# Optimization experiments

Hardware: AMD Instinct MI355X
Metric: run time of the kernel (lower is better)

The kernel has to match this reference:

```python
import jax, jax.numpy as jnp
import numpy as np

B, IN, H = 8192, 2048, 2048

def setup_inputs() -> dict:
    key = jax.random.key(0)
    k1, k2, k3, k4 = jax.random.split(key, 4)
    gate_bound = 1.0 / (IN + H)
    input_bound = 1.0 / IN
    return {
        "input": jax.random.normal(k1, (B, IN), dtype=jnp.float32),
        "state": jax.random.normal(k2, (B, H), dtype=jnp.float32),
        "gate_weights": jax.random.uniform(k3, (H, H + IN), dtype=jnp.float32, minval=-gate_bound, maxval=gate_bound),
        "gate_bias": jnp.full((H,), 0.5, dtype=jnp.float32),
        "weights_i": jax.random.uniform(k4, (H, IN), dtype=jnp.float32, minval=-input_bound, maxval=input_bound),
    }

def reference(input, state, gate_weights, gate_bias, weights_i):
    # concat_input: [B, IN+H]
    concat_input = jnp.concatenate([input, state], axis=1)
    # pre_gate_i = concat_input @ gate_weights.T + gate_bias : [B, H]
    pre_gate_i = jnp.einsum('bc,hc->bh', concat_input, gate_weights) + gate_bias
    # eval-mode noisy_hard_sigmoid == Hardtanh(0,1)
    gate_i = jnp.clip(pre_gate_i, 0.0, 1.0)
    # values_i = tanh(input @ weights_i.T) : [B, H]
    values_i = jnp.tanh(jnp.einsum('bi,hi->bh', input, weights_i))
    pre_h = state * (1.0 - gate_i) + values_i * gate_i
    # eval-mode noisy_relu == relu
    new_h = jax.nn.relu(pre_h)
    return (new_h, concat_input, pre_gate_i, gate_i, values_i, pre_h)
```

## Files before the change

### kernel.cpp

```cpp
#include <hip/hip_runtime.h>
#include <cstdint>
#include <cstddef>

#define B_SZ  8192
#define IN_SZ 2048
#define H_SZ  2048
#define KC_SZ 4096

typedef unsigned short ushort_t;
typedef __attribute__((ext_vector_type(8))) short bf16x8;
typedef __attribute__((ext_vector_type(4))) float floatx4;

__device__ __forceinline__ ushort_t f2bf(float f) {
  union { float f; unsigned u; } v; v.f = f;
  unsigned u = v.u;
  return (ushort_t)((u + 0x7FFFu + ((u >> 16) & 1u)) >> 16);
}

__device__ __forceinline__ void g2lds16(const void* g, void* l) {
  __builtin_amdgcn_global_load_lds(
      (const __attribute__((address_space(1))) unsigned int*)g,
      (__attribute__((address_space(3))) unsigned int*)l, 16, 0, 0);
}

__global__ void prep_concat(const float* __restrict__ in, const float* __restrict__ st,
                            float* __restrict__ cat, ushort_t* __restrict__ Abf) {
  size_t i4 = (size_t)blockIdx.x * blockDim.x + threadIdx.x;
  size_t row  = i4 >> 10;
  size_t col4 = i4 & 1023;
  float4 v;
  if (col4 < (IN_SZ / 4))
    v = ((const float4*)in)[row * (IN_SZ / 4) + col4];
  else
    v = ((const float4*)st)[row * (H_SZ / 4) + (col4 - IN_SZ / 4)];
  ((float4*)cat)[i4] = v;
  union { ushort_t u[4]; uint2 p; } pk;
  pk.u[0] = f2bf(v.x); pk.u[1] = f2bf(v.y); pk.u[2] = f2bf(v.z); pk.u[3] = f2bf(v.w);
  ((uint2*)Abf)[i4] = pk.p;
}

__global__ void prep_weights(const float* __restrict__ gw, const float* __restrict__ wi,
                             ushort_t* __restrict__ Wg, ushort_t* __restrict__ Wi) {
  size_t i4 = (size_t)blockIdx.x * blockDim.x + threadIdx.x;
  const size_t n1 = (size_t)H_SZ * KC_SZ / 4;
  union { ushort_t u[4]; uint2 p; } pk;
  if (i4 < n1) {
    float4 v = ((const float4*)gw)[i4];
    pk.u[0] = f2bf(v.x); pk.u[1] = f2bf(v.y); pk.u[2] = f2bf(v.z); pk.u[3] = f2bf(v.w);
    ((uint2*)Wg)[i4] = pk.p;
  } else {
    size_t j = i4 - n1;
    float4 v = ((const float4*)wi)[j];
    pk.u[0] = f2bf(v.x); pk.u[1] = f2bf(v.y); pk.u[2] = f2bf(v.z); pk.u[3] = f2bf(v.w);
    ((uint2*)Wi)[j] = pk.p;
  }
}

template <int EPI>
__global__ __launch_bounds__(256) void gemm_bt(
    const ushort_t* __restrict__ A, const ushort_t* __restrict__ W,
    int K, int lda, int ldw,
    float* __restrict__ o0, float* __restrict__ o1, float* __restrict__ o2,
    const float* __restrict__ x0, const float* __restrict__ x1) {
  constexpr int BM = 128, BN = 128, BK = 64;
  __shared__ __align__(16) ushort_t sA[BM * BK];
  __shared__ __align__(16) ushort_t sB[BN * BK];

  const int tid  = threadIdx.x;
  const int lane = tid & 63;
  const int quad = lane >> 4;
  const int l16  = lane & 15;
  const int wm = ((tid >> 6) >> 1) * 64;
  const int wn = ((tid >> 6) & 1) * 64;

  const int nTiles = H_SZ / BN;
  const int row0 = (blockIdx.x / nTiles) * BM;
  const int col0 = (blockIdx.x % nTiles) * BN;

  floatx4 acc[4][4] = {};

  const ushort_t* Ab = A + (size_t)row0 * lda;
  const ushort_t* Wb = W + (size_t)col0 * ldw;
  const int ldsbase = (tid & 192) * 8;

  for (int k0 = 0; k0 < K; k0 += BK) {
#pragma unroll
    for (int it = 0; it < 4; ++it) {
      int chunk = it * 256 + tid;
      int r = chunk >> 3;
      int c = (chunk & 7) << 3;
      g2lds16(Ab + (size_t)r * lda + (k0 + c), &sA[it * 2048 + ldsbase]);
    }
#pragma unroll
    for (int it = 0; it < 4; ++it) {
      int chunk = it * 256 + tid;
      int r = chunk >> 3;
      int c = (chunk & 7) << 3;
      g2lds16(Wb + (size_t)r * ldw + (k0 + c), &sB[it * 2048 + ldsbase]);
    }
    __syncthreads();
#pragma unroll
    for (int ks = 0; ks < BK; ks += 32) {
      bf16x8 af[4], bfr[4];
#pragma unroll
      for (int i = 0; i < 4; ++i)
        af[i] = *(const bf16x8*)&sA[(wm + i * 16 + l16) * BK + ks + quad * 8];
#pragma unroll
      for (int j = 0; j < 4; ++j)
        bfr[j] = *(const bf16x8*)&sB[(wn + j * 16 + l16) * BK + ks + quad * 8];
#pragma unroll
      for (int i = 0; i < 4; ++i)
#pragma unroll
        for (int j = 0; j < 4; ++j)
          acc[i][j] = __builtin_amdgcn_mfma_f32_16x16x32_bf16(af[i], bfr[j], acc[i][j], 0, 0, 0);
    }
    __syncthreads();
  }

  if (EPI == 0) {
    float bj[4];
#pragma unroll
    for (int j = 0; j < 4; ++j) bj[j] = x0[col0 + wn + j * 16 + l16];
#pragma unroll
    for (int i = 0; i < 4; ++i) {
      int rbase = row0 + wm + i * 16 + quad * 4;
#pragma unroll
      for (int j = 0; j < 4; ++j) {
        int col = col0 + wn + j * 16 + l16;
#pragma unroll
        for (int r = 0; r < 4; ++r) {
          size_t idx = (size_t)(rbase + r) * H_SZ + col;
          float pre = acc[i][j][r] + bj[j];
          o0[idx] = pre;
          o1[idx] = fminf(fmaxf(pre, 0.f), 1.f);
        }
      }
    }
  } else {
#pragma unroll
    for (int i = 0; i < 4; ++i) {
      int rbase = row0 + wm + i * 16 + quad * 4;
#pragma unroll
      for (int j = 0; j < 4; ++j) {
        int col = col0 + wn + j * 16 + l16;
#pragma unroll
        for (int r = 0; r < 4; ++r) {
          size_t idx = (size_t)(rbase + r) * H_SZ + col;
          float v  = tanhf(acc[i][j][r]);
          float g  = x0[idx];
          float s  = x1[idx];
          float ph = s * (1.f - g) + v * g;
          o0[idx] = v;
          o1[idx] = ph;
          o2[idx] = fmaxf(ph, 0.f);
        }
      }
    }
  }
}

__global__ void concat_only(const float* __restrict__ in, const float* __restrict__ st,
                            float* __restrict__ cat) {
  size_t i4 = (size_t)blockIdx.x * blockDim.x + threadIdx.x;
  size_t row = i4 >> 10, col4 = i4 & 1023;
  float4 v;
  if (col4 < (IN_SZ / 4))
    v = ((const float4*)in)[row * (IN_SZ / 4) + col4];
  else
    v = ((const float4*)st)[row * (H_SZ / 4) + (col4 - IN_SZ / 4)];
  ((float4*)cat)[i4] = v;
}

__global__ void naive_all(const float* __restrict__ in, const float* __restrict__ st,
                          const float* __restrict__ gw, const float* __restrict__ gb,
                          const float* __restrict__ wi,
                          float* __restrict__ new_h, float* __restrict__ pre_gate,
                          float* __restrict__ gate, float* __restrict__ values,
                          float* __restrict__ pre_h) {
  size_t idx = (size_t)blockIdx.x * blockDim.x + threadIdx.x;
  if (idx >= (size_t)B_SZ * H_SZ) return;
  int b = (int)(idx / H_SZ), h = (int)(idx % H_SZ);
  const float* wgr = gw + (size_t)h * KC_SZ;
  const float* wir = wi + (size_t)h * IN_SZ;
  const float* x = in + (size_t)b * IN_SZ;
  const float* s = st + (size_t)b * H_SZ;
  float ag = 0.f, av = 0.f;
  for (int c = 0; c < IN_SZ; ++c) { float a = x[c]; ag += a * wgr[c]; av += a * wir[c]; }
  for (int c = 0; c < H_SZ; ++c) ag += s[c] * wgr[IN_SZ + c];
  float pre = ag + gb[h];
  float g = fminf(fmaxf(pre, 0.f), 1.f);
  float v = tanhf(av);
  float ph = s[h] * (1.f - g) + v * g;
  pre_gate[idx] = pre; gate[idx] = g; values[idx] = v;
  pre_h[idx] = ph; new_h[idx] = fmaxf(ph, 0.f);
}

extern "C" void kernel_launch(void* const* d_in, const int* in_sizes, int n_in,
                              void* d_out, int out_size, void* d_ws, size_t ws_size,
                              hipStream_t stream) {
  const float* input = (const float*)d_in[0];
  const float* state = (const float*)d_in[1];
  const float* gw    = (const float*)d_in[2];
  const float* gb    = (const float*)d_in[3];
  const float* wi    = (const float*)d_in[4];

  float* out      = (float*)d_out;
  float* new_h    = out;
  float* cat      = new_h + (size_t)B_SZ * H_SZ;
  float* pre_gate = cat + (size_t)B_SZ * KC_SZ;
  float* gate     = pre_gate + (size_t)B_SZ * H_SZ;
  float* values   = gate + (size_t)B_SZ * H_SZ;
  float* pre_h    = values + (size_t)B_SZ * H_SZ;

  const size_t needA  = (size_t)B_SZ * KC_SZ * 2;
  const size_t needWg = (size_t)H_SZ * KC_SZ * 2;
  const size_t needWi = (size_t)H_SZ * IN_SZ * 2;
  if (ws_size >= needA + needWg + needWi) {
    ushort_t* Abf  = (ushort_t*)d_ws;
    ushort_t* Wgbf = Abf + (size_t)B_SZ * KC_SZ;
    ushort_t* Wibf = Wgbf + (size_t)H_SZ * KC_SZ;

    prep_concat<<<dim3((B_SZ * (size_t)KC_SZ / 4) / 256), dim3(256), 0, stream>>>(
        input, state, cat, Abf);
    prep_weights<<<dim3(((size_t)H_SZ * KC_SZ / 4 + (size_t)H_SZ * IN_SZ / 4) / 256),
                   dim3(256), 0, stream>>>(gw, wi, Wgbf, Wibf);

    const int grid = (B_SZ / 128) * (H_SZ / 128);
    gemm_bt<0><<<dim3(grid), dim3(256), 0, stream>>>(
        Abf, Wgbf, KC_SZ, KC_SZ, KC_SZ, pre_gate, gate, nullptr, gb, nullptr);
    gemm_bt<1><<<dim3(grid), dim3(256), 0, stream>>>(
        Abf, Wibf, IN_SZ, KC_SZ, IN_SZ, values, pre_h, new_h, gate, state);
  } else {
    concat_only<<<dim3((B_SZ * (size_t)KC_SZ / 4) / 256), dim3(256), 0, stream>>>(
        input, state, cat);
    naive_all<<<dim3((B_SZ * (size_t)H_SZ + 255) / 256), dim3(256), 0, stream>>>(
        input, state, gw, gb, wi, new_h, pre_gate, gate, values, pre_h);
  }
}
```

Before: 983.8 us.

## Fuse gate and value GEMMs into one kernel sharing A tiles

Replaces the two separate GEMM launches with one kernel that loads each A tile once and feeds both the gate and value weight tiles over the shared input K range, then continues with the gate weights over the state range. The whole epilogue (bias, clamp, tanh, blend, relu) runs from registers, so the gate array no longer has to be written and reread, and A is not streamed twice for the first half of K. To fit both accumulators the N tile drops from 128 to 64, which lowers per-block reuse of A and doubles the grid.

```diff
diff --git a/kernel.cpp b/kernel.cpp
--- a/kernel.cpp
+++ b/kernel.cpp
@@ -56,104 +56,134 @@
   }
 }
 
-template <int EPI>
-__global__ __launch_bounds__(256) void gemm_bt(
-    const ushort_t* __restrict__ A, const ushort_t* __restrict__ W,
-    int K, int lda, int ldw,
-    float* __restrict__ o0, float* __restrict__ o1, float* __restrict__ o2,
-    const float* __restrict__ x0, const float* __restrict__ x1) {
-  constexpr int BM = 128, BN = 128, BK = 64;
+__global__ __launch_bounds__(256) void gemm_fused(
+    const ushort_t* __restrict__ A, const ushort_t* __restrict__ Wg,
+    const ushort_t* __restrict__ Wi, const float* __restrict__ gb,
+    const float* __restrict__ st,
+    float* __restrict__ pre_gate, float* __restrict__ gate,
+    float* __restrict__ values, float* __restrict__ pre_h,
+    float* __restrict__ new_h) {
+  constexpr int BM = 128, BN = 64, BK = 64;
   __shared__ __align__(16) ushort_t sA[BM * BK];
-  __shared__ __align__(16) ushort_t sB[BN * BK];
+  __shared__ __align__(16) ushort_t sG[BN * BK];
+  __shared__ __align__(16) ushort_t sV[BN * BK];
 
   const int tid  = threadIdx.x;
   const int lane = tid & 63;
   const int quad = lane >> 4;
   const int l16  = lane & 15;
-  const int wm = ((tid >> 6) >> 1) * 64;
-  const int wn = ((tid >> 6) & 1) * 64;
+  const int wm   = ((tid >> 6) >> 1) * 64;
+  const int wn   = ((tid >> 6) & 1) * 32;
 
   const int nTiles = H_SZ / BN;
   const int row0 = (blockIdx.x / nTiles) * BM;
   const int col0 = (blockIdx.x % nTiles) * BN;
 
-  floatx4 acc[4][4] = {};
-
-  const ushort_t* Ab = A + (size_t)row0 * lda;
-  const ushort_t* Wb = W + (size_t)col0 * ldw;
+  floatx4 ag[4][2] = {};
+  floatx4 av[4][2] = {};
+
+  const ushort_t* Ab = A  + (size_t)row0 * KC_SZ;
+  const ushort_t* Gp = Wg + (size_t)col0 * KC_SZ;
+  const ushort_t* Vp = Wi + (size_t)col0 * IN_SZ;
   const int ldsbase = (tid & 192) * 8;
 
-  for (int k0 = 0; k0 < K; k0 += BK) {
+  int k0 = 0;
+  for (; k0 < IN_SZ; k0 += BK) {
 #pragma unroll
     for (int it = 0; it < 4; ++it) {
       int chunk = it * 256 + tid;
-      int r = chunk >> 3;
-      int c = (chunk & 7) << 3;
-      g2lds16(Ab + (size_t)r * lda + (k0 + c), &sA[it * 2048 + ldsbase]);
-    }
+      int r = chunk >> 3, c = (chunk & 7) << 3;
+      g2lds16(Ab + (size_t)r * KC_SZ + (k0 + c), &sA[it * 2048 + ldsbase]);
+    }
+#pragma unroll
+    for (int it = 0; it < 2; ++it) {
+      int chunk = it * 256 + tid;
+      int r = chunk >> 3, c = (chunk & 7) << 3;
+      g2lds16(Gp + (size_t)r * KC_SZ + (k0 + c), &sG[it * 2048 + ldsbase]);
+    }
+#pragma unroll
+    for (int it = 0; it < 2; ++it) {
+      int chunk = it * 256 + tid;
+      int r = chunk >> 3, c = (chunk & 7) << 3;
+      g2lds16(Vp + (size_t)r * IN_SZ + (k0 + c), &sV[it * 2048 + ldsbase]);
+    }
+    __syncthreads();
+#pragma unroll
+    for (int ks = 0; ks < BK; ks += 32) {
+      bf16x8 af[4], bg[2], bv[2];
+#pragma unroll
+      for (int i = 0; i < 4; ++i)
+        af[i] = *(const bf16x8*)&sA[(wm + i * 16 + l16) * BK + ks + quad * 8];
+#pragma unroll
+      for (int j = 0; j < 2; ++j) {
+        bg[j] = *(const bf16x8*)&sG[(wn + j * 16 + l16) * BK + ks + quad * 8];
+        bv[j] = *(const bf16x8*)&sV[(wn + j * 16 + l16) * BK + ks + quad * 8];
+      }
+#pragma unroll
+      for (int i = 0; i < 4; ++i)
+#pragma unroll
+        for (int j = 0; j < 2; ++j) {
+          ag[i][j] = __builtin_amdgcn_mfma_f32_16x16x32_bf16(af[i], bg[j], ag[i][j], 0, 0, 0);
+          av[i][j] = __builtin_amdgcn_mfma_f32_16x16x32_bf16(af[i], bv[j], av[i][j], 0, 0, 0);
+        }
+    }
+    __syncthreads();
+  }
+
+  for (; k0 < KC_SZ; k0 += BK) {
 #pragma unroll
     for (int it = 0; it < 4; ++it) {
       int chunk = it * 256 + tid;
-      int r = chunk >> 3;
-      int c = (chunk & 7) << 3;
-      g2lds16(Wb + (size_t)r * ldw + (k0 + c), &sB[it * 2048 + ldsbase]);
+      int r = chunk >> 3, c = (chunk & 7) << 3;
+      g2lds16(Ab + (size_t)r * KC_SZ + (k0 + c), &sA[it * 2048 + ldsbase]);
+    }
+#pragma unroll
+    for (int it = 0; it < 2; ++it) {
+      int chunk = it * 256 + tid;
+      int r = chunk >> 3, c = (chunk & 7) << 3;
+      g2lds16(Gp + (size_t)r * KC_SZ + (k0 + c), &sG[it * 2048 + ldsbase]);
     }
     __syncthreads();
 #pragma unroll
     for (int ks = 0; ks < BK; ks += 32) {
-      bf16x8 af[4], bfr[4];
+      bf16x8 af[4], bg[2];
 #pragma unroll
       for (int i = 0; i < 4; ++i)
         af[i] = *(const bf16x8*)&sA[(wm + i * 16 + l16) * BK + ks + quad * 8];
 #pragma unroll
-      for (int j = 0; j < 4; ++j)
-        bfr[j] = *(const bf16x8*)&sB[(wn + j * 16 + l16) * BK + ks + quad * 8];
-#pragma unroll
-      for (int i = 0; i < 4; ++i)
-#pragma unroll
-        for (int j = 0; j < 4; ++j)
-          acc[i][j] = __builtin_amdgcn_mfma_f32_16x16x32_bf16(af[i], bfr[j], acc[i][j], 0, 0, 0);
-    }
-    __syncthreads();
-  }
-
-  if (EPI == 0) {
-    float bj[4];
-#pragma unroll
-    for (int j = 0; j < 4; ++j) bj[j] = x0[col0 + wn + j * 16 + l16];
-#pragma unroll
-    for (int i = 0; i < 4; ++i) {
-      int rbase = row0 + wm + i * 16 + quad * 4;
-#pragma unroll
-      for (int j = 0; j < 4; ++j) {
-        int col = col0 + wn + j * 16 + l16;
-#pragma unroll
-        for (int r = 0; r < 4; ++r) {
-          size_t idx = (size_t)(rbase + r) * H_SZ + col;
-          float pre = acc[i][j][r] + bj[j];
-          o0[idx] = pre;
-          o1[idx] = fminf(fmaxf(pre, 0.f), 1.f);
-        }
-      }
-    }
-  } else {
-#pragma unroll
-    for (int i = 0; i < 4; ++i) {
-      int rbase = row0 + wm + i * 16 + quad * 4;
-#pragma unroll
-      for (int j = 0; j < 4; ++j) {
-        int col = col0 + wn + j * 16 + l16;
-#pragma unroll
-        for (int r = 0; r < 4; ++r) {
-          size_t idx = (size_t)(rbase + r) * H_SZ + col;
-          float v  = tanhf(acc[i][j][r]);
-          float g  = x0[idx];
-          float s  = x1[idx];
-          float ph = s * (1.f - g) + v * g;
-          o0[idx] = v;
-          o1[idx] = ph;
-          o2[idx] = fmaxf(ph, 0.f);
-        }
+      for (int j = 0; j < 2; ++j)
+        bg[j] = *(const bf16x8*)&sG[(wn + j * 16 + l16) * BK + ks + quad * 8];
+#pragma unroll
+      for (int i = 0; i < 4; ++i)
+#pragma unroll
+        for (int j = 0; j < 2; ++j)
+          ag[i][j] = __builtin_amdgcn_mfma_f32_16x16x32_bf16(af[i], bg[j], ag[i][j], 0, 0, 0);
+    }
+    __syncthreads();
+  }
+
+  float bj[2];
+#pragma unroll
+  for (int j = 0; j < 2; ++j) bj[j] = gb[col0 + wn + j * 16 + l16];
+#pragma unroll
+  for (int i = 0; i < 4; ++i) {
+    int rbase = row0 + wm + i * 16 + quad * 4;
+#pragma unroll
+    for (int j = 0; j < 2; ++j) {
+      int col = col0 + wn + j * 16 + l16;
+#pragma unroll
+      for (int r = 0; r < 4; ++r) {
+        size_t idx = (size_t)(rbase + r) * H_SZ + col;
+        float pre = ag[i][j][r] + bj[j];
+        float g   = fminf(fmaxf(pre, 0.f), 1.f);
+        float v   = tanhf(av[i][j][r]);
+        float s   = st[idx];
+        float ph  = s * (1.f - g) + v * g;
+        pre_gate[idx] = pre;
+        gate[idx]     = g;
+        values[idx]   = v;
+        pre_h[idx]    = ph;
+        new_h[idx]    = fmaxf(ph, 0.f);
       }
     }
   }
@@ -225,11 +255,9 @@
     prep_weights<<<dim3(((size_t)H_SZ * KC_SZ / 4 + (size_t)H_SZ * IN_SZ / 4) / 256),
                    dim3(256), 0, stream>>>(gw, wi, Wgbf, Wibf);
 
-    const int grid = (B_SZ / 128) * (H_SZ / 128);
-    gemm_bt<0><<<dim3(grid), dim3(256), 0, stream>>>(
-        Abf, Wgbf, KC_SZ, KC_SZ, KC_SZ, pre_gate, gate, nullptr, gb, nullptr);
-    gemm_bt<1><<<dim3(grid), dim3(256), 0, stream>>>(
-        Abf, Wibf, IN_SZ, KC_SZ, IN_SZ, values, pre_h, new_h, gate, state);
+    const int grid = (B_SZ / 128) * (H_SZ / 64);
+    gemm_fused<<<dim3(grid), dim3(256), 0, stream>>>(
+        Abf, Wgbf, Wibf, gb, state, pre_gate, gate, values, pre_h, new_h);
   } else {
     concat_only<<<dim3((B_SZ * (size_t)KC_SZ / 4) / 256), dim3(256), 0, stream>>>(
         input, state, cat);
```

Result: slower. 1.039 ms (+5.6%).

## Replace GEMM with 256x256 four-stage pipelined direct-to-LDS kernel with swizzle

Applied to the files above, without the earlier changes.

Replaces the 128x128 single-buffer GEMM with a 256x256 tile, 512-thread kernel that prefetches three K-slices ahead into a 4-deep LDS ring and uses fine-grained vmcnt waits instead of full syncthreads. Producer waves are split between A and B loads, LDS columns are XOR-swizzled to reduce bank conflicts, and setprio is raised around the MFMA bursts. The aim is to hide global load latency and raise per-block data reuse. In exchange it uses more registers (8x4 accumulators) and has a smaller grid of 256 blocks, which may under-fill the CUs.

```diff
diff --git a/kernel.cpp b/kernel.cpp
--- a/kernel.cpp
+++ b/kernel.cpp
@@ -57,64 +57,90 @@
 }
 
 template <int EPI>
-__global__ __launch_bounds__(256) void gemm_bt(
+__global__ __launch_bounds__(512, 2) void gemm_pipe(
     const ushort_t* __restrict__ A, const ushort_t* __restrict__ W,
     int K, int lda, int ldw,
     float* __restrict__ o0, float* __restrict__ o1, float* __restrict__ o2,
     const float* __restrict__ x0, const float* __restrict__ x1) {
-  constexpr int BM = 128, BN = 128, BK = 64;
-  __shared__ __align__(16) ushort_t sA[BM * BK];
-  __shared__ __align__(16) ushort_t sB[BN * BK];
+  constexpr int BM = 256, BN = 256, BK = 32;
+  constexpr int TILE_US = (BM + BN) * BK;
+  __shared__ __align__(16) ushort_t lds[4 * TILE_US];
 
   const int tid  = threadIdx.x;
   const int lane = tid & 63;
+  const int w    = tid >> 6;
   const int quad = lane >> 4;
   const int l16  = lane & 15;
-  const int wm = ((tid >> 6) >> 1) * 64;
-  const int wn = ((tid >> 6) & 1) * 64;
-
-  const int nTiles = H_SZ / BN;
-  const int row0 = (blockIdx.x / nTiles) * BM;
-  const int col0 = (blockIdx.x % nTiles) * BN;
-
-  floatx4 acc[4][4] = {};
-
-  const ushort_t* Ab = A + (size_t)row0 * lda;
-  const ushort_t* Wb = W + (size_t)col0 * ldw;
-  const int ldsbase = (tid & 192) * 8;
-
-  for (int k0 = 0; k0 < K; k0 += BK) {
-#pragma unroll
-    for (int it = 0; it < 4; ++it) {
-      int chunk = it * 256 + tid;
-      int r = chunk >> 3;
-      int c = (chunk & 7) << 3;
-      g2lds16(Ab + (size_t)r * lda + (k0 + c), &sA[it * 2048 + ldsbase]);
-    }
-#pragma unroll
-    for (int it = 0; it < 4; ++it) {
-      int chunk = it * 256 + tid;
-      int r = chunk >> 3;
-      int c = (chunk & 7) << 3;
-      g2lds16(Wb + (size_t)r * ldw + (k0 + c), &sB[it * 2048 + ldsbase]);
-    }
-    __syncthreads();
-#pragma unroll
-    for (int ks = 0; ks < BK; ks += 32) {
-      bf16x8 af[4], bfr[4];
-#pragma unroll
-      for (int i = 0; i < 4; ++i)
-        af[i] = *(const bf16x8*)&sA[(wm + i * 16 + l16) * BK + ks + quad * 8];
-#pragma unroll
-      for (int j = 0; j < 4; ++j)
-        bfr[j] = *(const bf16x8*)&sB[(wn + j * 16 + l16) * BK + ks + quad * 8];
-#pragma unroll
-      for (int i = 0; i < 4; ++i)
+  const int wm   = (w >> 2) * 128;
+  const int wn   = (w & 3) * 64;
+
+  const int row0 = (blockIdx.x >> 3) * BM;
+  const int col0 = (blockIdx.x & 7) * BN;
+
+  const int NT = K / BK;
+
+  const int rl = lane >> 2;
+  const int cl = ((lane & 3) << 3) ^ (((lane >> 5) & 1) << 4);
+  const bool isA = (w < 4);
+  const ushort_t* gbase = isA ? (A + (size_t)row0 * lda) : (W + (size_t)col0 * ldw);
+  const int ld = isA ? lda : ldw;
+  const int Rbase = (w & 3) * 4;
+  const size_t laneRowOff = (size_t)(Rbase * 16 + rl) * ld + cl;
+  const size_t ld16 = (size_t)ld * 16;
+  const int ldsSub = (isA ? 0 : BM * BK) + Rbase * 512;
+
+  floatx4 acc[8][4] = {};
+
+  for (int tt = 0; tt < 3; ++tt) {
+#pragma unroll
+    for (int q = 0; q < 4; ++q) {
+      const ushort_t* src = gbase + laneRowOff + (size_t)q * ld16 + (size_t)tt * BK;
+      g2lds16(src, &lds[(tt & 3) * TILE_US + ldsSub + q * 512]);
+    }
+  }
+  asm volatile("s_waitcnt vmcnt(8)" ::: "memory");
+  __builtin_amdgcn_sched_barrier(0);
+  __builtin_amdgcn_s_barrier();
+
+  const int cp = (quad << 3) ^ ((l16 >> 3) << 4);
+  const int fragBase = l16 * 32 + cp;
+
+  for (int t = 0; t < NT; ++t) {
+    const ushort_t* bufA = &lds[(t & 3) * TILE_US];
+    const ushort_t* bufB = bufA + BM * BK;
+    const bool pf = (t + 3 < NT);
+    bf16x8 bfr[4];
+#pragma unroll
+    for (int p = 0; p < 4; ++p) {
+      if (pf) {
+        const ushort_t* src = gbase + laneRowOff + (size_t)p * ld16 + (size_t)(t + 3) * BK;
+        g2lds16(src, &lds[((t + 3) & 3) * TILE_US + ldsSub + p * 512]);
+      }
+      if (p == 0) {
 #pragma unroll
         for (int j = 0; j < 4; ++j)
-          acc[i][j] = __builtin_amdgcn_mfma_f32_16x16x32_bf16(af[i], bfr[j], acc[i][j], 0, 0, 0);
-    }
-    __syncthreads();
+          bfr[j] = *(const bf16x8*)&bufB[((wn >> 4) + j) * 512 + fragBase];
+      }
+      bf16x8 a0 = *(const bf16x8*)&bufA[((wm >> 4) + 2 * p) * 512 + fragBase];
+      bf16x8 a1 = *(const bf16x8*)&bufA[((wm >> 4) + 2 * p + 1) * 512 + fragBase];
+      __builtin_amdgcn_s_setprio(1);
+#pragma unroll
+      for (int j = 0; j < 4; ++j) {
+        acc[2 * p][j]     = __builtin_amdgcn_mfma_f32_16x16x32_bf16(a0, bfr[j], acc[2 * p][j], 0, 0, 0);
+        acc[2 * p + 1][j] = __builtin_amdgcn_mfma_f32_16x16x32_bf16(a1, bfr[j], acc[2 * p + 1][j], 0, 0, 0);
+      }
+      __builtin_amdgcn_s_setprio(0);
+      if (p < 3) {
+        __builtin_amdgcn_s_barrier();
+      } else {
+        const int rem = NT - 1 - t;
+        if (rem >= 3)      asm volatile("s_waitcnt vmcnt(8)" ::: "memory");
+        else if (rem == 2) asm volatile("s_waitcnt vmcnt(4)" ::: "memory");
+        else if (rem == 1) asm volatile("s_waitcnt vmcnt(0)" ::: "memory");
+        __builtin_amdgcn_sched_barrier(0);
+        __builtin_amdgcn_s_barrier();
+      }
+    }
   }
 
   if (EPI == 0) {
@@ -122,7 +148,7 @@
 #pragma unroll
     for (int j = 0; j < 4; ++j) bj[j] = x0[col0 + wn + j * 16 + l16];
 #pragma unroll
-    for (int i = 0; i < 4; ++i) {
+    for (int i = 0; i < 8; ++i) {
       int rbase = row0 + wm + i * 16 + quad * 4;
 #pragma unroll
       for (int j = 0; j < 4; ++j) {
@@ -138,7 +164,7 @@
     }
   } else {
 #pragma unroll
-    for (int i = 0; i < 4; ++i) {
+    for (int i = 0; i < 8; ++i) {
       int rbase = row0 + wm + i * 16 + quad * 4;
 #pragma unroll
       for (int j = 0; j < 4; ++j) {
@@ -225,10 +251,10 @@
     prep_weights<<<dim3(((size_t)H_SZ * KC_SZ / 4 + (size_t)H_SZ * IN_SZ / 4) / 256),
                    dim3(256), 0, stream>>>(gw, wi, Wgbf, Wibf);
 
-    const int grid = (B_SZ / 128) * (H_SZ / 128);
-    gemm_bt<0><<<dim3(grid), dim3(256), 0, stream>>>(
+    const int grid = (B_SZ / 256) * (H_SZ / 256);
+    gemm_pipe<0><<<dim3(grid), dim3(512), 0, stream>>>(
         Abf, Wgbf, KC_SZ, KC_SZ, KC_SZ, pre_gate, gate, nullptr, gb, nullptr);
-    gemm_bt<1><<<dim3(grid), dim3(256), 0, stream>>>(
+    gemm_pipe<1><<<dim3(grid), dim3(512), 0, stream>>>(
         Abf, Wibf, IN_SZ, KC_SZ, IN_SZ, values, pre_h, new_h, gate, state);
   } else {
     concat_only<<<dim3((B_SZ * (size_t)KC_SZ / 4) / 256), dim3(256), 0, stream>>>(
```

After: 871.9 us. 1.13x faster.
